# Performance work log

Measured on AMD Instinct MI355X. Metric: run time of the kernel, lower is better.

## Reference

```python
import jax, jax.numpy as jnp
import numpy as np

THRESHOLD = 0.5
NEG_POS_RATIO = 3
ALPHA = 1.0
B, P, C, O = 128, 8732, 21, 32


def xy_to_cxcy(xy):
    return jnp.concatenate([(xy[..., 2:] + xy[..., :2]) / 2, xy[..., 2:] - xy[..., :2]], axis=-1)


def cxcy_to_xy(cxcy):
    return jnp.concatenate([cxcy[..., :2] - cxcy[..., 2:] / 2, cxcy[..., :2] + cxcy[..., 2:] / 2], axis=-1)


def cxcy_to_gcxgcy(cxcy, priors_cxcy):
    g_cxcy = (cxcy[..., :2] - priors_cxcy[..., :2]) / (priors_cxcy[..., 2:] / 10.0)
    g_wh = jnp.log(cxcy[..., 2:] / priors_cxcy[..., 2:]) * 5.0
    return jnp.concatenate([g_cxcy, g_wh], axis=-1)


def find_jaccard_overlap(set1, set2):
    # set1: [O,4] xy, set2: [P,4] xy -> [O,P]
    lo = jnp.maximum(set1[:, None, :2], set2[None, :, :2])
    hi = jnp.minimum(set1[:, None, 2:], set2[None, :, 2:])
    inter = jnp.prod(jnp.clip(hi - lo, 0.0), axis=-1)
    a1 = jnp.prod(set1[:, 2:] - set1[:, :2], axis=-1)
    a2 = jnp.prod(set2[:, 2:] - set2[:, :2], axis=-1)
    union = a1[:, None] + a2[None, :] - inter
    return inter / union


def setup_inputs() -> dict:
    key = jax.random.key(0)
    k0, k1, k2, k3, k4, k5, k6 = jax.random.split(key, 7)
    predicted_locs = jax.random.normal(k0, (B, P, 4), jnp.float32)
    predicted_scores = jax.random.normal(k1, (B, P, C), jnp.float32)
    centers = jax.random.uniform(k2, (B, O, 2), jnp.float32, 0.2, 0.8)
    sizes = jax.random.uniform(k3, (B, O, 2), jnp.float32, 0.05, 0.3)
    boxes = jnp.concatenate([centers - sizes / 2, centers + sizes / 2], axis=-1)
    labels = jax.random.randint(k4, (B, O), 0, C)
    p_c = jax.random.uniform(k5, (P, 2), jnp.float32, 0.05, 0.95)
    p_wh = jax.random.uniform(k6, (P, 2), jnp.float32, 0.05, 0.5)
    priors_cxcy = jnp.concatenate([p_c, p_wh], axis=-1)
    return {"predicted_locs": predicted_locs, "predicted_scores": predicted_scores,
            "boxes": boxes, "labels": labels, "priors_cxcy": priors_cxcy}


def reference(predicted_locs, predicted_scores, boxes, labels, priors_cxcy):
    priors_xy = cxcy_to_xy(priors_cxcy)

    def match_one(boxes_i, labels_i):
        overlap = find_jaccard_overlap(boxes_i, priors_xy)           # [O,P]
        overlap_for_each_prior = jnp.max(overlap, axis=0)            # [P]
        object_for_each_prior = jnp.argmax(overlap, axis=0)          # [P]
        prior_for_each_object = jnp.argmax(overlap, axis=1)          # [O]
        object_for_each_prior = object_for_each_prior.at[prior_for_each_object].set(jnp.arange(O))
        overlap_for_each_prior = overlap_for_each_prior.at[prior_for_each_object].set(1.0)
        label_for_each_prior = labels_i[object_for_each_prior]
        label_for_each_prior = jnp.where(overlap_for_each_prior < THRESHOLD, 0, label_for_each_prior)
        true_locs_i = cxcy_to_gcxgcy(xy_to_cxcy(boxes_i[object_for_each_prior]), priors_cxcy)
        return label_for_each_prior, true_locs_i

    true_classes, true_locs = jax.vmap(match_one)(boxes, labels)     # [B,P], [B,P,4]

    positive = true_classes != 0                                     # [B,P]
    n_positives = jnp.sum(positive, axis=1)                          # [B]
    n_pos_total = jnp.sum(n_positives)

    # L1Loss (mean over selected positive elements, 4 per prior)
    abs_diff = jnp.abs(predicted_locs - true_locs)                   # [B,P,4]
    loc_loss = jnp.sum(abs_diff * positive[..., None]) / (n_pos_total.astype(jnp.float32) * 4.0)

    # per-element cross-entropy
    log_p = jax.nn.log_softmax(predicted_scores, axis=-1)            # [B,P,C]
    conf_loss_all = -jnp.take_along_axis(log_p, true_classes[..., None], axis=-1)[..., 0]  # [B,P]

    conf_loss_pos_sum = jnp.sum(jnp.where(positive, conf_loss_all, 0.0))
    conf_loss_neg = jnp.where(positive, 0.0, conf_loss_all)
    conf_loss_neg_sorted = -jnp.sort(-conf_loss_neg, axis=1)         # descending
    n_hard = NEG_POS_RATIO * n_positives                             # [B]
    hard_mask = jnp.arange(P)[None, :] < n_hard[:, None]             # [B,P]
    conf_loss_hard_neg_sum = jnp.sum(jnp.where(hard_mask, conf_loss_neg_sorted, 0.0))

    conf_loss = (conf_loss_hard_neg_sum + conf_loss_pos_sum) / n_pos_total.astype(jnp.float32)
    return conf_loss + ALPHA * loc_loss
```

## Files before the change

### kernel.cpp

```cpp
#include <hip/hip_runtime.h>
#include <hip/hip_bf16.h>

#define NB 128
#define NP 8732
#define NO 32
#define NC 21
#define NCHUNK 35


__device__ __forceinline__ float wave64_fmax_u(float m) {
    int v;
    v = __builtin_amdgcn_update_dpp(__float_as_int(m), __float_as_int(m), 0x111, 0xf, 0xf, false);
    m = fmaxf(m, __int_as_float(v));
    v = __builtin_amdgcn_update_dpp(__float_as_int(m), __float_as_int(m), 0x112, 0xf, 0xf, false);
    m = fmaxf(m, __int_as_float(v));
    v = __builtin_amdgcn_update_dpp(__float_as_int(m), __float_as_int(m), 0x114, 0xf, 0xf, false);
    m = fmaxf(m, __int_as_float(v));
    v = __builtin_amdgcn_update_dpp(__float_as_int(m), __float_as_int(m), 0x118, 0xf, 0xf, false);
    m = fmaxf(m, __int_as_float(v));
    v = __builtin_amdgcn_update_dpp(__float_as_int(m), __float_as_int(m), 0x142, 0xf, 0xf, false);
    m = fmaxf(m, __int_as_float(v));
    v = __builtin_amdgcn_update_dpp(__float_as_int(m), __float_as_int(m), 0x143, 0xf, 0xf, false);
    m = fmaxf(m, __int_as_float(v));
    return __int_as_float(__builtin_amdgcn_readlane(__float_as_int(m), 63));
}

__device__ __forceinline__ int wave64_imin_u(int m) {
    int v;
    v = __builtin_amdgcn_update_dpp(m, m, 0x111, 0xf, 0xf, false); m = v < m ? v : m;
    v = __builtin_amdgcn_update_dpp(m, m, 0x112, 0xf, 0xf, false); m = v < m ? v : m;
    v = __builtin_amdgcn_update_dpp(m, m, 0x114, 0xf, 0xf, false); m = v < m ? v : m;
    v = __builtin_amdgcn_update_dpp(m, m, 0x118, 0xf, 0xf, false); m = v < m ? v : m;
    v = __builtin_amdgcn_update_dpp(m, m, 0x142, 0xf, 0xf, false); m = v < m ? v : m;
    v = __builtin_amdgcn_update_dpp(m, m, 0x143, 0xf, 0xf, false); m = v < m ? v : m;
    return __builtin_amdgcn_readlane(m, 63);
}

__global__ __launch_bounds__(256) void k_obj(const float* __restrict__ boxes,
                                             const float* __restrict__ priors,
                                             int* __restrict__ pfor) {
    __shared__ float4 spr[1024];
    int b = blockIdx.y;
    int tid = threadIdx.x, lane = tid & 63, wid = tid >> 6;
    int o0 = blockIdx.x * 8 + wid * 2;

    float4 bx0 = ((const float4*)boxes)[b * NO + o0];
    float4 bx1 = ((const float4*)boxes)[b * NO + o0 + 1];
    float a10 = (bx0.z - bx0.x) * (bx0.w - bx0.y);
    float a11 = (bx1.z - bx1.x) * (bx1.w - bx1.y);

    float bv0 = -1.0f, bv1 = -1.0f;
    int   bp0 = 0,     bp1 = 0;

    for (int c0 = 0; c0 < NP; c0 += 1024) {
        int n = NP - c0; if (n > 1024) n = 1024;
        __syncthreads();
        for (int i = tid; i < n; i += 256)
            spr[i] = ((const float4*)priors)[c0 + i];
        __syncthreads();
#pragma unroll 4
        for (int i = lane; i < n; i += 64) {
            float4 pr = spr[i];
            float x1 = pr.x - pr.z * 0.5f, y1 = pr.y - pr.w * 0.5f;
            float x2 = pr.x + pr.z * 0.5f, y2 = pr.y + pr.w * 0.5f;
            float pa = (x2 - x1) * (y2 - y1);
            int p = c0 + i;
            {
                float lx = fmaxf(bx0.x, x1), ly = fmaxf(bx0.y, y1);
                float hx = fminf(bx0.z, x2), hy = fminf(bx0.w, y2);
                float inter = fmaxf(hx - lx, 0.0f) * fmaxf(hy - ly, 0.0f);
                float iou = inter / (a10 + pa - inter);
                if (iou > bv0) { bv0 = iou; bp0 = p; }
            }
            {
                float lx = fmaxf(bx1.x, x1), ly = fmaxf(bx1.y, y1);
                float hx = fminf(bx1.z, x2), hy = fminf(bx1.w, y2);
                float inter = fmaxf(hx - lx, 0.0f) * fmaxf(hy - ly, 0.0f);
                float iou = inter / (a11 + pa - inter);
                if (iou > bv1) { bv1 = iou; bp1 = p; }
            }
        }
    }
    float m0 = wave64_fmax_u(bv0);
    int mp0 = wave64_imin_u((bv0 == m0) ? bp0 : 0x7FFFFFFF);
    float m1 = wave64_fmax_u(bv1);
    int mp1 = wave64_imin_u((bv1 == m1) ? bp1 : 0x7FFFFFFF);
    if (lane == 0) {
        pfor[b * NO + o0]     = mp0;
        pfor[b * NO + o0 + 1] = mp1;
    }
}

__global__ __launch_bounds__(256) void k_loss(const float* __restrict__ plocs,
                                              const float* __restrict__ scores,
                                              const float* __restrict__ boxes,
                                              const int* __restrict__ labels,
                                              const float* __restrict__ priors,
                                              const int* __restrict__ pfor,
                                              float* __restrict__ confneg,
                                              int* __restrict__ pnp,
                                              double* __restrict__ pd0,
                                              double* __restrict__ pd1,
                                              int* __restrict__ donecnt) {
    __shared__ float srow[256 * NC];
    __shared__ float4 sbox[NO];
    __shared__ int spfl[NO];
    int b = blockIdx.y;
    int p0 = blockIdx.x * 256;
    int cnt = NP - p0; if (cnt > 256) cnt = 256;
    int nf4 = cnt * NC / 4;
    const float4* src4 = (const float4*)(scores + ((size_t)b * NP + p0) * NC);
    for (int i = threadIdx.x; i < nf4; i += 256)
        ((float4*)srow)[i] = src4[i];
    if (threadIdx.x < NO) {
        sbox[threadIdx.x] = ((const float4*)boxes)[b * NO + threadIdx.x];
        spfl[threadIdx.x] = pfor[b * NO + threadIdx.x];
    }
    __syncthreads();

    int p = p0 + threadIdx.x;
    float posconf = 0.0f, locpart = 0.0f;
    int isp = 0;

    if (p < NP) {
        float4 pr = ((const float4*)priors)[p];
        float px1 = pr.x - pr.z * 0.5f, py1 = pr.y - pr.w * 0.5f;
        float px2 = pr.x + pr.z * 0.5f, py2 = pr.y + pr.w * 0.5f;
        float pa  = (px2 - px1) * (py2 - py1);

        float bestv = -1.0f; int besto = 0;
#pragma unroll
        for (int o = 0; o < NO; ++o) {
            float4 bx = sbox[o];
            float a1 = (bx.z - bx.x) * (bx.w - bx.y);
            float lx = fmaxf(bx.x, px1), ly = fmaxf(bx.y, py1);
            float hx = fminf(bx.z, px2), hy = fminf(bx.w, py2);
            float inter = fmaxf(hx - lx, 0.0f) * fmaxf(hy - ly, 0.0f);
            float iou = inter / (a1 + pa - inter);
            if (iou > bestv) { bestv = iou; besto = o; }
        }
        int obj = besto;
        int mat = bestv >= 0.5f ? 1 : 0;
#pragma unroll
        for (int o = 0; o < NO; ++o)
            if (spfl[o] == p) { obj = o; mat = 1; }
        int lbl = mat ? labels[b * NO + obj] : 0;

        const float* s = srow + threadIdx.x * NC;
        float m = s[0];
#pragma unroll
        for (int c = 1; c < NC; ++c) m = fmaxf(m, s[c]);
        float sum = 0.0f;
#pragma unroll
        for (int c = 0; c < NC; ++c) sum += __expf(s[c] - m);
        float conf = m + __logf(sum) - s[lbl];

        if (lbl != 0) {
            isp = 1;
            posconf = conf;
            float4 bx = sbox[obj];
            float cx = (bx.x + bx.z) * 0.5f, cy = (bx.y + bx.w) * 0.5f;
            float w = bx.z - bx.x, h = bx.w - bx.y;
            float gx = (cx - pr.x) / (pr.z * 0.1f);
            float gy = (cy - pr.y) / (pr.w * 0.1f);
            float gw = __logf(w / pr.z) * 5.0f;
            float gh = __logf(h / pr.w) * 5.0f;
            float4 pl = ((const float4*)plocs)[(size_t)b * NP + p];
            locpart = fabsf(pl.x - gx) + fabsf(pl.y - gy) +
                      fabsf(pl.z - gw) + fabsf(pl.w - gh);
        }
        confneg[(size_t)b * NP + p] = isp ? 0.0f : conf;
    }

    for (int s = 32; s > 0; s >>= 1) {
        posconf += __shfl_xor(posconf, s, 64);
        locpart += __shfl_xor(locpart, s, 64);
        isp     += __shfl_xor(isp, s, 64);
    }
    __shared__ float w0[4], w1[4];
    __shared__ int wc[4];
    int wid = threadIdx.x >> 6, lane = threadIdx.x & 63;
    if (lane == 0) { w0[wid] = posconf; w1[wid] = locpart; wc[wid] = isp; }
    __syncthreads();
    if (threadIdx.x == 0) {
        int pb = b * NCHUNK + blockIdx.x;
        pd0[pb] = (double)(w0[0] + w0[1] + w0[2] + w0[3]);
        pd1[pb] = (double)(w1[0] + w1[1] + w1[2] + w1[3]);
        pnp[pb] = wc[0] + wc[1] + wc[2] + wc[3];
        if (pb == 0) *donecnt = 0;
    }
}

__global__ __launch_bounds__(1024) void k_topk(const float* __restrict__ confneg,
                                               const int* __restrict__ pnp,
                                               const double* __restrict__ pd0,
                                               const double* __restrict__ pd1,
                                               int* __restrict__ snp,
                                               double* __restrict__ sums,
                                               int* __restrict__ donecnt,
                                               float* __restrict__ out) {
    __shared__ int    si2[2][16];
    __shared__ int    siw[16];
    __shared__ double sdd[16];
    __shared__ int    sk;
    int tid = threadIdx.x, b = blockIdx.x;
    int lane = tid & 63, wid = tid >> 6;

    if (wid == 0) {
        int np_ = 0; double d0 = 0.0, d1 = 0.0;
        if (lane < NCHUNK) {
            int pb = b * NCHUNK + lane;
            np_ = pnp[pb]; d0 = pd0[pb]; d1 = pd1[pb];
        }
        for (int s = 32; s > 0; s >>= 1) {
            np_ += __shfl_xor(np_, s, 64);
            d0  += __shfl_xor(d0, s, 64);
            d1  += __shfl_xor(d1, s, 64);
        }
        if (lane == 0) {
            int k = np_ * 3; if (k > NP) k = NP;
            sk = k;
            snp[b] = np_;
            sums[b * 3 + 1] = d0;
            sums[b * 3 + 2] = d1;
        }
    }

    const float* src = confneg + (size_t)b * NP;
    float val[9];
#pragma unroll
    for (int j = 0; j < 9; ++j) {
        int i = tid + j * 1024;
        val[j] = (i < NP) ? src[i] : 0.0f;
    }
    __syncthreads();
    int k = sk;

    double hn = 0.0;
    if (k > 0) {
        unsigned T = 0;
        int par = 0;
        for (int bit = 30; bit >= 0; --bit) {
            unsigned cand = T | (1u << bit);
            int cnt = 0;
#pragma unroll
            for (int j = 0; j < 9; ++j)
                cnt += __popcll(__ballot(__float_as_uint(val[j]) >= cand));
            if (lane == 0) si2[par][wid] = cnt;
            __syncthreads();
            int t = 0;
#pragma unroll
            for (int w = 0; w < 16; ++w) t += si2[par][w];
            par ^= 1;
            if (t >= k) T = cand;
        }

        int cgt = 0;
        double sgt = 0.0;
#pragma unroll
        for (int j = 0; j < 9; ++j) {
            unsigned u = __float_as_uint(val[j]);
            if (u > T) { cgt++; sgt += (double)val[j]; }
        }
        for (int s = 32; s > 0; s >>= 1) {
            cgt += __shfl_xor(cgt, s, 64);
            sgt += __shfl_xor(sgt, s, 64);
        }
        if (lane == 0) { siw[wid] = cgt; sdd[wid] = sgt; }
        __syncthreads();
        if (tid == 0) {
            int cg = 0; double sg = 0.0;
            for (int w = 0; w < 16; ++w) { cg += siw[w]; sg += sdd[w]; }
            hn = sg + (double)(k - cg) * (double)__uint_as_float(T);
        }
    }
    if (tid == 0) sums[b * 3 + 0] = hn;

    __shared__ int samlast;
    if (tid == 0) {
        __threadfence();
        int prev = atomicAdd(donecnt, 1);
        samlast = (prev == NB - 1) ? 1 : 0;
    }
    __syncthreads();
    if (!samlast) return;
    __threadfence();

    double hnn = 0.0, pc = 0.0, lc = 0.0, npd = 0.0;
    if (tid < NB) {
        hnn = atomicAdd(&sums[tid * 3 + 0], 0.0);
        pc  = atomicAdd(&sums[tid * 3 + 1], 0.0);
        lc  = atomicAdd(&sums[tid * 3 + 2], 0.0);
        npd = (double)atomicAdd((int*)&snp[tid], 0);
    }
    for (int s = 32; s > 0; s >>= 1) {
        hnn += __shfl_xor(hnn, s, 64);
        pc  += __shfl_xor(pc, s, 64);
        lc  += __shfl_xor(lc, s, 64);
        npd += __shfl_xor(npd, s, 64);
    }
    __shared__ double sfin[4][2];
    if (lane == 0 && wid < 2) {
        sfin[0][wid] = hnn; sfin[1][wid] = pc; sfin[2][wid] = lc; sfin[3][wid] = npd;
    }
    __syncthreads();
    if (tid == 0) {
        double H  = sfin[0][0] + sfin[0][1];
        double P  = sfin[1][0] + sfin[1][1];
        double L  = sfin[2][0] + sfin[2][1];
        double nt = sfin[3][0] + sfin[3][1];
        out[0] = (float)((H + P) / nt + L / (nt * 4.0));
    }
}

extern "C" void kernel_launch(void* const* d_in, const int* in_sizes, int n_in,
                              void* d_out, int out_size, void* d_ws, size_t ws_size,
                              hipStream_t stream) {
    const float* plocs  = (const float*)d_in[0];
    const float* scores = (const float*)d_in[1];
    const float* boxes  = (const float*)d_in[2];
    const int*   labels = (const int*)d_in[3];
    const float* priors = (const float*)d_in[4];
    float* out = (float*)d_out;

    char* ws = (char*)d_ws;
    int*    pfor    = (int*)ws;
    double* pd0     = (double*)(ws + 16384);
    double* pd1     = (double*)(ws + 52224);
    int*    pnp     = (int*)(ws + 88064);
    int*    snp     = (int*)(ws + 105984);
    double* sums    = (double*)(ws + 106496);
    int*    donecnt = (int*)(ws + 109568);
    float*  confneg = (float*)(ws + 109824);

    hipLaunchKernelGGL(k_obj, dim3(NO / 8, NB), dim3(256), 0, stream,
                       boxes, priors, pfor);
    hipLaunchKernelGGL(k_loss, dim3(NCHUNK, NB), dim3(256), 0, stream,
                       plocs, scores, boxes, labels, priors, pfor,
                       confneg, pnp, pd0, pd1, donecnt);
    hipLaunchKernelGGL(k_topk, dim3(NB), dim3(1024), 0, stream,
                       confneg, pnp, pd0, pd1, snp, sums, donecnt, out);
}
```

Before: 227.6 us.

## Load score rows directly into registers, drop LDS staging, precompute box data

```diff
diff --git a/kernel.cpp b/kernel.cpp
--- a/kernel.cpp
+++ b/kernel.cpp
@@ -1,5 +1,4 @@
 #include <hip/hip_runtime.h>
-#include <hip/hip_bf16.h>
 
 #define NB 128
 #define NP 8732
@@ -102,23 +101,37 @@
                                               double* __restrict__ pd0,
                                               double* __restrict__ pd1,
                                               int* __restrict__ donecnt) {
-    __shared__ float srow[256 * NC];
     __shared__ float4 sbox[NO];
-    __shared__ int spfl[NO];
+    __shared__ float  sa1[NO];
+    __shared__ int    slbl[NO];
+    __shared__ int    sfp[NO], sfo[NO];
+    __shared__ int    snf;
     int b = blockIdx.y;
     int p0 = blockIdx.x * 256;
-    int cnt = NP - p0; if (cnt > 256) cnt = 256;
-    int nf4 = cnt * NC / 4;
-    const float4* src4 = (const float4*)(scores + ((size_t)b * NP + p0) * NC);
-    for (int i = threadIdx.x; i < nf4; i += 256)
-        ((float4*)srow)[i] = src4[i];
-    if (threadIdx.x < NO) {
-        sbox[threadIdx.x] = ((const float4*)boxes)[b * NO + threadIdx.x];
-        spfl[threadIdx.x] = pfor[b * NO + threadIdx.x];
-    }
-    __syncthreads();
-
-    int p = p0 + threadIdx.x;
+    int tid = threadIdx.x;
+
+    if (tid < NO) {
+        float4 bx = ((const float4*)boxes)[b * NO + tid];
+        sbox[tid] = bx;
+        sa1[tid]  = (bx.z - bx.x) * (bx.w - bx.y);
+        slbl[tid] = labels[b * NO + tid];
+    }
+    if (tid < 64) {
+        int f = -1, inr = 0;
+        if (tid < NO) {
+            f = pfor[b * NO + tid];
+            inr = (f >= p0) && (f < p0 + 256);
+        }
+        unsigned long long mask = __ballot(inr);
+        if (inr) {
+            int rank = __popcll(mask & ((1ull << tid) - 1));
+            sfp[rank] = f; sfo[rank] = tid;
+        }
+        if (tid == 0) snf = __popcll(mask);
+    }
+    __syncthreads();
+
+    int p = p0 + tid;
     float posconf = 0.0f, locpart = 0.0f;
     int isp = 0;
 
@@ -132,28 +145,35 @@
 #pragma unroll
         for (int o = 0; o < NO; ++o) {
             float4 bx = sbox[o];
-            float a1 = (bx.z - bx.x) * (bx.w - bx.y);
             float lx = fmaxf(bx.x, px1), ly = fmaxf(bx.y, py1);
             float hx = fminf(bx.z, px2), hy = fminf(bx.w, py2);
             float inter = fmaxf(hx - lx, 0.0f) * fmaxf(hy - ly, 0.0f);
-            float iou = inter / (a1 + pa - inter);
+            float iou = inter / (sa1[o] + pa - inter);
             if (iou > bestv) { bestv = iou; besto = o; }
         }
         int obj = besto;
         int mat = bestv >= 0.5f ? 1 : 0;
-#pragma unroll
-        for (int o = 0; o < NO; ++o)
-            if (spfl[o] == p) { obj = o; mat = 1; }
-        int lbl = mat ? labels[b * NO + obj] : 0;
-
-        const float* s = srow + threadIdx.x * NC;
+        int nf = snf;
+        for (int i = 0; i < nf; ++i)
+            if (sfp[i] == p) { obj = sfo[i]; mat = 1; }
+        int lbl = mat ? slbl[obj] : 0;
+
+        const float* srow = scores + ((size_t)b * NP + p) * NC;
+        const float4* r4 = (const float4*)srow;
+        float4 q0 = r4[0], q1 = r4[1], q2 = r4[2], q3 = r4[3], q4 = r4[4];
+        float s[NC] = {q0.x, q0.y, q0.z, q0.w, q1.x, q1.y, q1.z, q1.w,
+                       q2.x, q2.y, q2.z, q2.w, q3.x, q3.y, q3.z, q3.w,
+                       q4.x, q4.y, q4.z, q4.w, srow[20]};
         float m = s[0];
 #pragma unroll
         for (int c = 1; c < NC; ++c) m = fmaxf(m, s[c]);
-        float sum = 0.0f;
-#pragma unroll
-        for (int c = 0; c < NC; ++c) sum += __expf(s[c] - m);
-        float conf = m + __logf(sum) - s[lbl];
+        float sum = 0.0f, sl = s[0];
+#pragma unroll
+        for (int c = 0; c < NC; ++c) {
+            sum += __expf(s[c] - m);
+            if (c > 0) sl = (lbl == c) ? s[c] : sl;
+        }
+        float conf = m + __logf(sum) - sl;
 
         if (lbl != 0) {
             isp = 1;
@@ -179,10 +199,10 @@
     }
     __shared__ float w0[4], w1[4];
     __shared__ int wc[4];
-    int wid = threadIdx.x >> 6, lane = threadIdx.x & 63;
+    int wid = tid >> 6, lane = tid & 63;
     if (lane == 0) { w0[wid] = posconf; w1[wid] = locpart; wc[wid] = isp; }
     __syncthreads();
-    if (threadIdx.x == 0) {
+    if (tid == 0) {
         int pb = b * NCHUNK + blockIdx.x;
         pd0[pb] = (double)(w0[0] + w0[1] + w0[2] + w0[3]);
         pd1[pb] = (double)(w1[0] + w1[1] + w1[2] + w1[3]);
```

Result: no change. 225.0 us (-1.1%).
